# Optimization experiments

Measured on AMD Instinct MI355X. Metric: run time of the kernel, lower is better.

Reference implementation:

```python
import jax, jax.numpy as jnp
import numpy as np

B, C, W, H = 8, 256, 64, 64


def _conv1x1(x, w, b):
    # 1x1 conv == per-pixel channel GEMM. x: [B,C,W,H], w: [O,C], b: [O]
    return jnp.einsum('oc,bchw->bohw', w, x) + b[None, :, None, None]


def setup_inputs() -> dict:
    key = jax.random.key(0)
    ks = jax.random.split(key, 9)
    s = 1.0 / np.sqrt(C)
    return {
        'queries': jax.random.normal(ks[0], (B, C, W, H), dtype=jnp.float32),
        'keys': jax.random.normal(ks[1], (B, C, W, H), dtype=jnp.float32),
        'mask': jax.random.uniform(ks[2], (B, 1, W, H), dtype=jnp.float32),
        'Wq': jax.random.normal(ks[3], (C, C), dtype=jnp.float32) * s,
        'bq': jax.random.normal(ks[4], (C,), dtype=jnp.float32) * 0.01,
        'Wk': jax.random.normal(ks[5], (C, C), dtype=jnp.float32) * s,
        'bk': jax.random.normal(ks[6], (C,), dtype=jnp.float32) * 0.01,
        'Wv': jax.random.normal(ks[7], (C, C), dtype=jnp.float32) * s,
        'bv': jax.random.normal(ks[8], (C,), dtype=jnp.float32) * 0.01,
    }


def reference(queries, keys, mask, Wq, bq, Wk, bk, Wv, bv):
    b, c, w, h = queries.shape
    n = w * h
    q = _conv1x1(queries, Wq, bq).reshape(b, c, n)   # [B,C,N]
    k = _conv1x1(keys, Wk, bk).reshape(b, c, n)      # [B,C,N]
    v = _conv1x1(keys, Wv, bv).reshape(b, c, n)      # [B,C,N]
    # mask spatial size equals feature size -> interpolate(scale_factor=1) is identity
    m = mask.reshape(b, n)                            # [B,N]
    # scores[b,i,j] = <q_i, k_j>; torch's repeated mask multiplies row i by mask[i]
    scores = jnp.einsum('bcq,bck->bqk', q, k) * m[:, :, None]
    attn_w = jax.nn.softmax(scores, axis=-1)          # softmax over key dim
    attn = jnp.einsum('bqk,bck->bcq', attn_w, v).reshape(b, c, w, h)
    return queries * mask + (1.0 - mask) * attn
```

## Files before the change

### kernel.cpp

```cpp
#include <hip/hip_runtime.h>

typedef __attribute__((ext_vector_type(8))) _Float16 half8;
typedef __attribute__((ext_vector_type(4))) _Float16 half4;
typedef __attribute__((ext_vector_type(4))) float f32x4;

#define CDIM 256
#define NDIM 4096
#define MFMAH(a, b, c) __builtin_amdgcn_mfma_f32_16x16x32_f16((a), (b), (c), 0, 0, 0)

__global__ void cast_w_kernel(const float* __restrict__ Wq,
                              const float* __restrict__ Wk,
                              const float* __restrict__ Wv,
                              _Float16* __restrict__ Wc) {
  int t = blockIdx.x * 256 + threadIdx.x;
  int mat = t >> 14;
  int idx = (t & 16383) * 4;
  const float* W = (mat == 0) ? Wq : (mat == 1 ? Wk : Wv);
  float4 w = *(const float4*)(W + idx);
  half4 h = {(_Float16)w.x, (_Float16)w.y, (_Float16)w.z, (_Float16)w.w};
  *(half4*)(Wc + mat * 65536 + idx) = h;
}

__global__ __launch_bounds__(256, 2) void proj_kernel(
    const float* __restrict__ queries, const float* __restrict__ keys,
    const _Float16* __restrict__ Wc,
    const float* __restrict__ bq, const float* __restrict__ bk,
    const float* __restrict__ bv,
    _Float16* __restrict__ Qh, _Float16* __restrict__ Kh,
    _Float16* __restrict__ Vh)
{
  const int z = blockIdx.z, p = z >> 3, b = z & 7;
  const float* __restrict__ X = (p == 0) ? queries : keys;
  const _Float16* __restrict__ W = Wc + p * 65536;
  const float* __restrict__ bias = (p == 0) ? bq : (p == 1 ? bk : bv);
  const int n0 = blockIdx.x * 128;

  __shared__ __align__(16) _Float16 Xs[128][264];

  const int tid = threadIdx.x;
  const int wv = tid >> 6, lane = tid & 63, l16 = lane & 15, quad = lane >> 4;

#pragma unroll
  for (int it = 0; it < 32; ++it) {
    int id = tid + it * 256;
    int c = id >> 5, n4 = id & 31;
    float4 x = *(const float4*)&X[((size_t)(b * CDIM + c)) * NDIM + n0 + n4 * 4];
    Xs[n4 * 4 + 0][c] = (_Float16)x.x;
    Xs[n4 * 4 + 1][c] = (_Float16)x.y;
    Xs[n4 * 4 + 2][c] = (_Float16)x.z;
    Xs[n4 * 4 + 3][c] = (_Float16)x.w;
  }
  __syncthreads();

  f32x4 acc[4][8];
#pragma unroll
  for (int og = 0; og < 4; ++og)
#pragma unroll
    for (int ng = 0; ng < 8; ++ng) acc[og][ng] = (f32x4){0.f, 0.f, 0.f, 0.f};

#pragma unroll
  for (int kc = 0; kc < 8; ++kc) {
    half8 wf[4], xf[8];
#pragma unroll
    for (int og = 0; og < 4; ++og)
      wf[og] = *(const half8*)(W + (wv * 64 + og * 16 + l16) * CDIM + kc * 32 + quad * 8);
#pragma unroll
    for (int ng = 0; ng < 8; ++ng)
      xf[ng] = *(const half8*)&Xs[ng * 16 + l16][kc * 32 + quad * 8];
#pragma unroll
    for (int og = 0; og < 4; ++og)
#pragma unroll
      for (int ng = 0; ng < 8; ++ng)
        acc[og][ng] = MFMAH(wf[og], xf[ng], acc[og][ng]);
  }

#pragma unroll
  for (int og = 0; og < 4; ++og) {
    float4 b4 = *(const float4*)&bias[wv * 64 + og * 16 + quad * 4];
#pragma unroll
    for (int ng = 0; ng < 8; ++ng) {
      const int n = n0 + ng * 16 + l16;
      if (p == 2) {
#pragma unroll
        for (int r = 0; r < 4; ++r) {
          int o = wv * 64 + og * 16 + quad * 4 + r;
          float y = acc[og][ng][r] + ((const float*)&b4)[r];
          Vh[((size_t)(b * CDIM + o)) * NDIM + n] = (_Float16)y;
        }
      } else {
        half4 h4;
#pragma unroll
        for (int r = 0; r < 4; ++r)
          h4[r] = (_Float16)(acc[og][ng][r] + ((const float*)&b4)[r]);
        size_t idx = ((size_t)(b * NDIM + n)) * CDIM + wv * 64 + og * 16 + quad * 4;
        if (p == 0) *(half4*)&Qh[idx] = h4;
        else        *(half4*)&Kh[idx] = h4;
      }
    }
  }
}

__global__ __launch_bounds__(256, 2) void attn_kernel(
    const float* __restrict__ queries, const float* __restrict__ mask,
    const _Float16* __restrict__ Qh, const _Float16* __restrict__ Kh,
    const _Float16* __restrict__ Vh, float* __restrict__ out)
{
  const int blk = blockIdx.x, b = blk & 7, it = blk >> 3;
  const int i0 = it * 64;

  __shared__ __align__(16) _Float16 Ks[64][264];
  __shared__ __align__(16) _Float16 Ps[2][64][72];
  __shared__ __align__(16) float Al[2][64];
  __shared__ __align__(16) float Li[64];

  const int tid = threadIdx.x;
  const int wv = tid >> 6, lane = tid & 63, l16 = lane & 15, quad = lane >> 4;

  half8 qf[8];
  {
    const size_t qrow = ((size_t)(b * NDIM + i0 + wv * 16 + l16)) * CDIM;
#pragma unroll
    for (int kc = 0; kc < 8; ++kc)
      qf[kc] = *(const half8*)(Qh + qrow + kc * 32 + quad * 8);
  }
  const float mval = mask[(size_t)b * NDIM + i0 + wv * 16 + l16];
  float m_run = -1e30f, l_run = 0.f;

  f32x4 O[4][4];
#pragma unroll
  for (int g = 0; g < 4; ++g)
#pragma unroll
    for (int cg = 0; cg < 4; ++cg) O[g][cg] = (f32x4){0.f, 0.f, 0.f, 0.f};

  const _Float16* __restrict__ Kb = Kh + (size_t)b * NDIM * CDIM;
  const _Float16* __restrict__ Vw = Vh + ((size_t)(b * CDIM + wv * 64)) * NDIM;

  for (int jt = 0; jt < 64; ++jt) {
    const int j0 = jt * 64;
    const int pb = jt & 1;
#pragma unroll
    for (int it2 = 0; it2 < 8; ++it2) {
      int id = tid + it2 * 256;
      int j = id >> 5, c8 = id & 31;
      *(uint4*)&Ks[j][c8 * 8] = *(const uint4*)(Kb + (size_t)(j0 + j) * CDIM + c8 * 8);
    }
    half8 vf[2][4];
#pragma unroll
    for (int kk = 0; kk < 2; ++kk)
#pragma unroll
      for (int cg = 0; cg < 4; ++cg)
        vf[kk][cg] = *(const half8*)(Vw + (size_t)(cg * 16 + l16) * NDIM + j0 + kk * 32 + quad * 8);
    __syncthreads();

    f32x4 s[4];
#pragma unroll
    for (int js = 0; js < 4; ++js) s[js] = (f32x4){0.f, 0.f, 0.f, 0.f};
#pragma unroll
    for (int kc = 0; kc < 8; ++kc) {
#pragma unroll
      for (int js = 0; js < 4; ++js) {
        half8 kf = *(const half8*)&Ks[js * 16 + l16][kc * 32 + quad * 8];
        s[js] = MFMAH(kf, qf[kc], s[js]);
      }
    }

    float a[16];
    float mx = -1e30f;
#pragma unroll
    for (int js = 0; js < 4; ++js)
#pragma unroll
      for (int r = 0; r < 4; ++r) {
        float v = s[js][r] * mval;
        a[js * 4 + r] = v;
        mx = fmaxf(mx, v);
      }
    mx = fmaxf(mx, __shfl_xor(mx, 16));
    mx = fmaxf(mx, __shfl_xor(mx, 32));
    const float mnew = fmaxf(m_run, mx);
    const float alpha = __expf(m_run - mnew);
    m_run = mnew;
    float psum = 0.f;
#pragma unroll
    for (int js = 0; js < 4; ++js) {
      float p0 = __expf(a[js * 4 + 0] - mnew);
      float p1 = __expf(a[js * 4 + 1] - mnew);
      float p2 = __expf(a[js * 4 + 2] - mnew);
      float p3 = __expf(a[js * 4 + 3] - mnew);
      psum += (p0 + p1) + (p2 + p3);
      half4 hp = {(_Float16)p0, (_Float16)p1, (_Float16)p2, (_Float16)p3};
      *(half4*)&Ps[pb][wv * 16 + l16][js * 16 + quad * 4] = hp;
    }
    psum += __shfl_xor(psum, 16);
    psum += __shfl_xor(psum, 32);
    l_run = l_run * alpha + psum;
    if (quad == 0) Al[pb][wv * 16 + l16] = alpha;
    __syncthreads();

    f32x4 av[4];
#pragma unroll
    for (int g = 0; g < 4; ++g) av[g] = *(const f32x4*)&Al[pb][g * 16 + quad * 4];
#pragma unroll
    for (int g = 0; g < 4; ++g)
#pragma unroll
      for (int cg = 0; cg < 4; ++cg)
#pragma unroll
        for (int r = 0; r < 4; ++r) O[g][cg][r] *= av[g][r];
#pragma unroll
    for (int kk = 0; kk < 2; ++kk) {
      half8 pa[4];
#pragma unroll
      for (int g = 0; g < 4; ++g)
        pa[g] = *(const half8*)&Ps[pb][g * 16 + l16][kk * 32 + quad * 8];
#pragma unroll
      for (int g = 0; g < 4; ++g)
#pragma unroll
        for (int cg = 0; cg < 4; ++cg)
          O[g][cg] = MFMAH(pa[g], vf[kk][cg], O[g][cg]);
    }
  }

  if (quad == 0) Li[wv * 16 + l16] = 1.0f / l_run;
  __syncthreads();
#pragma unroll
  for (int g = 0; g < 4; ++g) {
    f32x4 li4 = *(const f32x4*)&Li[g * 16 + quad * 4];
    const int i = i0 + g * 16 + quad * 4;
    float4 m4 = *(const float4*)&mask[(size_t)b * NDIM + i];
#pragma unroll
    for (int cg = 0; cg < 4; ++cg) {
      const int c = wv * 64 + cg * 16 + l16;
      const size_t base = ((size_t)(b * CDIM + c)) * NDIM + i;
      float4 q4 = *(const float4*)(queries + base);
      float4 o4;
      o4.x = q4.x * m4.x + (1.f - m4.x) * (O[g][cg][0] * li4[0]);
      o4.y = q4.y * m4.y + (1.f - m4.y) * (O[g][cg][1] * li4[1]);
      o4.z = q4.z * m4.z + (1.f - m4.z) * (O[g][cg][2] * li4[2]);
      o4.w = q4.w * m4.w + (1.f - m4.w) * (O[g][cg][3] * li4[3]);
      *(float4*)(out + base) = o4;
    }
  }
}

extern "C" void kernel_launch(void* const* d_in, const int* in_sizes, int n_in,
                              void* d_out, int out_size, void* d_ws, size_t ws_size,
                              hipStream_t stream) {
  const float* queries = (const float*)d_in[0];
  const float* keys    = (const float*)d_in[1];
  const float* mask    = (const float*)d_in[2];
  const float* Wq = (const float*)d_in[3];
  const float* bq = (const float*)d_in[4];
  const float* Wk = (const float*)d_in[5];
  const float* bk = (const float*)d_in[6];
  const float* Wv = (const float*)d_in[7];
  const float* bv = (const float*)d_in[8];
  float* out = (float*)d_out;

  const size_t elems = (size_t)8 * NDIM * CDIM;
  _Float16* Qh = (_Float16*)d_ws;
  _Float16* Kh = Qh + elems;
  _Float16* Vh = Kh + elems;
  _Float16* Wc = Vh + elems;

  cast_w_kernel<<<dim3(192), 256, 0, stream>>>(Wq, Wk, Wv, Wc);
  proj_kernel<<<dim3(32, 1, 24), 256, 0, stream>>>(
      queries, keys, Wc, bq, bk, bv, Qh, Kh, Vh);
  attn_kernel<<<dim3(512), 256, 0, stream>>>(
      queries, mask, Qh, Kh, Vh, out);
}
```

Before: 331.1 us.

## Switch attention to 32x32x16 MFMA with 2x2 wave split over query and key tiles

Restructures the attention kernel so each wave computes a 32x32 score tile (query half by key half) with 32x32x16 MFMAs. Per-wave row max and sum go through shared memory and are merged across the two key halves, and P is rescaled by each half's factor before the PV MFMA. The softmax uses exp2 with log2e folded into the mask. The intent is fewer MFMA instructions and less redundant K LDS traffic per wave. In exchange it adds extra shared-memory reductions, fp16 rescaling of P, and a scalar, less coalesced output store.

```diff
diff --git a/kernel.cpp b/kernel.cpp
--- a/kernel.cpp
+++ b/kernel.cpp
@@ -3,10 +3,12 @@
 typedef __attribute__((ext_vector_type(8))) _Float16 half8;
 typedef __attribute__((ext_vector_type(4))) _Float16 half4;
 typedef __attribute__((ext_vector_type(4))) float f32x4;
+typedef __attribute__((ext_vector_type(16))) float f32x16;
 
 #define CDIM 256
 #define NDIM 4096
 #define MFMAH(a, b, c) __builtin_amdgcn_mfma_f32_16x16x32_f16((a), (b), (c), 0, 0, 0)
+#define MFMA32(a, b, c) __builtin_amdgcn_mfma_f32_32x32x16_f16((a), (b), (c), 0, 0, 0)
 
 __global__ void cast_w_kernel(const float* __restrict__ Wq,
                               const float* __restrict__ Wk,
@@ -110,27 +112,35 @@
 
   __shared__ __align__(16) _Float16 Ks[64][264];
   __shared__ __align__(16) _Float16 Ps[2][64][72];
-  __shared__ __align__(16) float Al[2][64];
-  __shared__ __align__(16) float Li[64];
+  __shared__ __align__(16) float Mx[2][2][64];
+  __shared__ __align__(16) float Ls[2][2][64];
 
   const int tid = threadIdx.x;
-  const int wv = tid >> 6, lane = tid & 63, l16 = lane & 15, quad = lane >> 4;
-
-  half8 qf[8];
+  const int wv = tid >> 6, lane = tid & 63;
+  const int l32 = lane & 31, hk = lane >> 5;
+  const int wi = wv >> 1, wj = wv & 1;
+
+  const float LOG2E = 1.44269504088896f;
+
+  half8 qf[16];
   {
-    const size_t qrow = ((size_t)(b * NDIM + i0 + wv * 16 + l16)) * CDIM;
-#pragma unroll
-    for (int kc = 0; kc < 8; ++kc)
-      qf[kc] = *(const half8*)(Qh + qrow + kc * 32 + quad * 8);
-  }
-  const float mval = mask[(size_t)b * NDIM + i0 + wv * 16 + l16];
-  float m_run = -1e30f, l_run = 0.f;
-
-  f32x4 O[4][4];
-#pragma unroll
-  for (int g = 0; g < 4; ++g)
-#pragma unroll
-    for (int cg = 0; cg < 4; ++cg) O[g][cg] = (f32x4){0.f, 0.f, 0.f, 0.f};
+    const size_t qrow = ((size_t)(b * NDIM + i0 + wi * 32 + l32)) * CDIM;
+#pragma unroll
+    for (int kc = 0; kc < 16; ++kc)
+      qf[kc] = *(const half8*)(Qh + qrow + kc * 16 + hk * 8);
+  }
+
+  const float mvalL = mask[(size_t)b * NDIM + i0 + wi * 32 + l32] * LOG2E;
+  float m_run[2] = {-1e30f, -1e30f};
+  float l_run[2] = {0.f, 0.f};
+
+  f32x16 O[2][2];
+#pragma unroll
+  for (int t = 0; t < 2; ++t)
+#pragma unroll
+    for (int ct = 0; ct < 2; ++ct)
+#pragma unroll
+      for (int r = 0; r < 16; ++r) O[t][ct][r] = 0.f;
 
   const _Float16* __restrict__ Kb = Kh + (size_t)b * NDIM * CDIM;
   const _Float16* __restrict__ Vw = Vh + ((size_t)(b * CDIM + wv * 64)) * NDIM;
@@ -139,104 +149,98 @@
     const int j0 = jt * 64;
     const int pb = jt & 1;
 #pragma unroll
-    for (int it2 = 0; it2 < 8; ++it2) {
-      int id = tid + it2 * 256;
+    for (int st = 0; st < 8; ++st) {
+      int id = tid + st * 256;
       int j = id >> 5, c8 = id & 31;
       *(uint4*)&Ks[j][c8 * 8] = *(const uint4*)(Kb + (size_t)(j0 + j) * CDIM + c8 * 8);
     }
-    half8 vf[2][4];
-#pragma unroll
-    for (int kk = 0; kk < 2; ++kk)
-#pragma unroll
-      for (int cg = 0; cg < 4; ++cg)
-        vf[kk][cg] = *(const half8*)(Vw + (size_t)(cg * 16 + l16) * NDIM + j0 + kk * 32 + quad * 8);
+    half8 va[2][4];
+#pragma unroll
+    for (int ct = 0; ct < 2; ++ct)
+#pragma unroll
+      for (int js = 0; js < 4; ++js)
+        va[ct][js] = *(const half8*)(Vw + (size_t)(ct * 32 + l32) * NDIM + j0 + js * 16 + hk * 8);
     __syncthreads();
 
-    f32x4 s[4];
-#pragma unroll
-    for (int js = 0; js < 4; ++js) s[js] = (f32x4){0.f, 0.f, 0.f, 0.f};
-#pragma unroll
-    for (int kc = 0; kc < 8; ++kc) {
-#pragma unroll
-      for (int js = 0; js < 4; ++js) {
-        half8 kf = *(const half8*)&Ks[js * 16 + l16][kc * 32 + quad * 8];
-        s[js] = MFMAH(kf, qf[kc], s[js]);
-      }
+    f32x16 s0, s1;
+#pragma unroll
+    for (int r = 0; r < 16; ++r) { s0[r] = 0.f; s1[r] = 0.f; }
+#pragma unroll
+    for (int kc = 0; kc < 16; kc += 2) {
+      half8 kfa = *(const half8*)&Ks[wj * 32 + l32][kc * 16 + hk * 8];
+      half8 kfb = *(const half8*)&Ks[wj * 32 + l32][(kc + 1) * 16 + hk * 8];
+      s0 = MFMA32(kfa, qf[kc], s0);
+      s1 = MFMA32(kfb, qf[kc + 1], s1);
     }
 
     float a[16];
-    float mx = -1e30f;
-#pragma unroll
-    for (int js = 0; js < 4; ++js)
-#pragma unroll
-      for (int r = 0; r < 4; ++r) {
-        float v = s[js][r] * mval;
-        a[js * 4 + r] = v;
-        mx = fmaxf(mx, v);
-      }
-    mx = fmaxf(mx, __shfl_xor(mx, 16));
-    mx = fmaxf(mx, __shfl_xor(mx, 32));
-    const float mnew = fmaxf(m_run, mx);
-    const float alpha = __expf(m_run - mnew);
-    m_run = mnew;
+    float lm = -1e30f;
+#pragma unroll
+    for (int r = 0; r < 16; ++r) {
+      a[r] = (s0[r] + s1[r]) * mvalL;
+      lm = fmaxf(lm, a[r]);
+    }
+    lm = fmaxf(lm, __shfl_xor(lm, 32));
     float psum = 0.f;
 #pragma unroll
-    for (int js = 0; js < 4; ++js) {
-      float p0 = __expf(a[js * 4 + 0] - mnew);
-      float p1 = __expf(a[js * 4 + 1] - mnew);
-      float p2 = __expf(a[js * 4 + 2] - mnew);
-      float p3 = __expf(a[js * 4 + 3] - mnew);
+    for (int rq = 0; rq < 4; ++rq) {
+      float p0 = exp2f(a[rq * 4 + 0] - lm);
+      float p1 = exp2f(a[rq * 4 + 1] - lm);
+      float p2 = exp2f(a[rq * 4 + 2] - lm);
+      float p3 = exp2f(a[rq * 4 + 3] - lm);
       psum += (p0 + p1) + (p2 + p3);
       half4 hp = {(_Float16)p0, (_Float16)p1, (_Float16)p2, (_Float16)p3};
-      *(half4*)&Ps[pb][wv * 16 + l16][js * 16 + quad * 4] = hp;
-    }
-    psum += __shfl_xor(psum, 16);
+      *(half4*)&Ps[pb][wi * 32 + l32][wj * 32 + rq * 8 + hk * 4] = hp;
+    }
     psum += __shfl_xor(psum, 32);
-    l_run = l_run * alpha + psum;
-    if (quad == 0) Al[pb][wv * 16 + l16] = alpha;
+    if (hk == 0) {
+      Mx[pb][wj][wi * 32 + l32] = lm;
+      Ls[pb][wj][wi * 32 + l32] = psum;
+    }
     __syncthreads();
 
-    f32x4 av[4];
-#pragma unroll
-    for (int g = 0; g < 4; ++g) av[g] = *(const f32x4*)&Al[pb][g * 16 + quad * 4];
-#pragma unroll
-    for (int g = 0; g < 4; ++g)
-#pragma unroll
-      for (int cg = 0; cg < 4; ++cg)
-#pragma unroll
-        for (int r = 0; r < 4; ++r) O[g][cg][r] *= av[g][r];
-#pragma unroll
-    for (int kk = 0; kk < 2; ++kk) {
-      half8 pa[4];
-#pragma unroll
-      for (int g = 0; g < 4; ++g)
-        pa[g] = *(const half8*)&Ps[pb][g * 16 + l16][kk * 32 + quad * 8];
-#pragma unroll
-      for (int g = 0; g < 4; ++g)
-#pragma unroll
-        for (int cg = 0; cg < 4; ++cg)
-          O[g][cg] = MFMAH(pa[g], vf[kk][cg], O[g][cg]);
-    }
-  }
-
-  if (quad == 0) Li[wv * 16 + l16] = 1.0f / l_run;
-  __syncthreads();
-#pragma unroll
-  for (int g = 0; g < 4; ++g) {
-    f32x4 li4 = *(const f32x4*)&Li[g * 16 + quad * 4];
-    const int i = i0 + g * 16 + quad * 4;
-    float4 m4 = *(const float4*)&mask[(size_t)b * NDIM + i];
-#pragma unroll
-    for (int cg = 0; cg < 4; ++cg) {
-      const int c = wv * 64 + cg * 16 + l16;
-      const size_t base = ((size_t)(b * CDIM + c)) * NDIM + i;
-      float4 q4 = *(const float4*)(queries + base);
-      float4 o4;
-      o4.x = q4.x * m4.x + (1.f - m4.x) * (O[g][cg][0] * li4[0]);
-      o4.y = q4.y * m4.y + (1.f - m4.y) * (O[g][cg][1] * li4[1]);
-      o4.z = q4.z * m4.z + (1.f - m4.z) * (O[g][cg][2] * li4[2]);
-      o4.w = q4.w * m4.w + (1.f - m4.w) * (O[g][cg][3] * li4[3]);
-      *(float4*)(out + base) = o4;
+#pragma unroll
+    for (int t = 0; t < 2; ++t) {
+      const int irow = t * 32 + l32;
+      const float mx0 = Mx[pb][0][irow];
+      const float mx1 = Mx[pb][1][irow];
+      const float mnew = fmaxf(m_run[t], fmaxf(mx0, mx1));
+      const float alpha = exp2f(m_run[t] - mnew);
+      const float f0 = exp2f(mx0 - mnew);
+      const float f1 = exp2f(mx1 - mnew);
+      l_run[t] = l_run[t] * alpha + Ls[pb][0][irow] * f0 + Ls[pb][1][irow] * f1;
+      m_run[t] = mnew;
+#pragma unroll
+      for (int ct = 0; ct < 2; ++ct)
+#pragma unroll
+        for (int r = 0; r < 16; ++r) O[t][ct][r] *= alpha;
+      const _Float16 hf0 = (_Float16)f0, hf1 = (_Float16)f1;
+#pragma unroll
+      for (int js = 0; js < 4; ++js) {
+        half8 pf = *(const half8*)&Ps[pb][irow][js * 16 + hk * 8];
+        const _Float16 sc = (js < 2) ? hf0 : hf1;
+#pragma unroll
+        for (int e = 0; e < 8; ++e) pf[e] *= sc;
+#pragma unroll
+        for (int ct = 0; ct < 2; ++ct)
+          O[t][ct] = MFMA32(va[ct][js], pf, O[t][ct]);
+      }
+    }
+  }
+
+#pragma unroll
+  for (int t = 0; t < 2; ++t) {
+    const int i = i0 + t * 32 + l32;
+    const float mv = mask[(size_t)b * NDIM + i];
+    const float rl = (1.f - mv) / l_run[t];
+#pragma unroll
+    for (int ct = 0; ct < 2; ++ct) {
+#pragma unroll
+      for (int r = 0; r < 16; ++r) {
+        const int c = wv * 64 + ct * 32 + (r & 3) + 8 * (r >> 2) + 4 * hk;
+        const size_t base = ((size_t)(b * CDIM + c)) * NDIM + i;
+        out[base] = queries[base] * mv + rl * O[t][ct][r];
+      }
     }
   }
 }
```

Result: slower. 348.9 us (+5.4%).

## Prefetch next K tile into registers and swizzle projection LDS staging

Applied to the files above, without the earlier changes.

In the attention loop, the next 64-row K tile is loaded into registers while the current tile is written to shared memory and consumed, so global-load latency overlaps compute. The last iteration wraps around and prefetches tile 0 redundantly. In the projection kernel, the input is staged with four channels per thread and stored as half4 vectors into an XOR-swizzled LDS layout, replacing scalar transposing stores to cut LDS bank conflicts. The reads use the matching swizzle. The register prefetch adds 32 VGPRs per thread, which may lower occupancy.

```diff
diff --git a/kernel.cpp b/kernel.cpp
--- a/kernel.cpp
+++ b/kernel.cpp
@@ -41,14 +41,24 @@
   const int wv = tid >> 6, lane = tid & 63, l16 = lane & 15, quad = lane >> 4;
 
 #pragma unroll
-  for (int it = 0; it < 32; ++it) {
+  for (int it = 0; it < 8; ++it) {
     int id = tid + it * 256;
-    int c = id >> 5, n4 = id & 31;
-    float4 x = *(const float4*)&X[((size_t)(b * CDIM + c)) * NDIM + n0 + n4 * 4];
-    Xs[n4 * 4 + 0][c] = (_Float16)x.x;
-    Xs[n4 * 4 + 1][c] = (_Float16)x.y;
-    Xs[n4 * 4 + 2][c] = (_Float16)x.z;
-    Xs[n4 * 4 + 3][c] = (_Float16)x.w;
+    int n4 = id & 31, c0 = (id >> 5) * 4;
+    const float* Xp = &X[((size_t)(b * CDIM + c0)) * NDIM + n0 + n4 * 4];
+    float4 x0 = *(const float4*)(Xp);
+    float4 x1 = *(const float4*)(Xp + NDIM);
+    float4 x2 = *(const float4*)(Xp + 2 * NDIM);
+    float4 x3 = *(const float4*)(Xp + 3 * NDIM);
+    const int cs = c0 ^ ((n4 & 7) << 3);
+    half4 h;
+    h = (half4){(_Float16)x0.x, (_Float16)x1.x, (_Float16)x2.x, (_Float16)x3.x};
+    *(half4*)&Xs[n4 * 4 + 0][cs] = h;
+    h = (half4){(_Float16)x0.y, (_Float16)x1.y, (_Float16)x2.y, (_Float16)x3.y};
+    *(half4*)&Xs[n4 * 4 + 1][cs] = h;
+    h = (half4){(_Float16)x0.z, (_Float16)x1.z, (_Float16)x2.z, (_Float16)x3.z};
+    *(half4*)&Xs[n4 * 4 + 2][cs] = h;
+    h = (half4){(_Float16)x0.w, (_Float16)x1.w, (_Float16)x2.w, (_Float16)x3.w};
+    *(half4*)&Xs[n4 * 4 + 3][cs] = h;
   }
   __syncthreads();
 
@@ -65,8 +75,10 @@
     for (int og = 0; og < 4; ++og)
       wf[og] = *(const half8*)(W + (wv * 64 + og * 16 + l16) * CDIM + kc * 32 + quad * 8);
 #pragma unroll
-    for (int ng = 0; ng < 8; ++ng)
-      xf[ng] = *(const half8*)&Xs[ng * 16 + l16][kc * 32 + quad * 8];
+    for (int ng = 0; ng < 8; ++ng) {
+      const int row = ng * 16 + l16;
+      xf[ng] = *(const half8*)&Xs[row][(kc * 32 + quad * 8) ^ (((row >> 2) & 7) << 3)];
+    }
 #pragma unroll
     for (int og = 0; og < 4; ++og)
 #pragma unroll
@@ -135,14 +147,29 @@
   const _Float16* __restrict__ Kb = Kh + (size_t)b * NDIM * CDIM;
   const _Float16* __restrict__ Vw = Vh + ((size_t)(b * CDIM + wv * 64)) * NDIM;
 
+  uint4 kreg[8];
+#pragma unroll
+  for (int st = 0; st < 8; ++st) {
+    int id = tid + st * 256;
+    int j = id >> 5, c8 = id & 31;
+    kreg[st] = *(const uint4*)(Kb + (size_t)j * CDIM + c8 * 8);
+  }
+
   for (int jt = 0; jt < 64; ++jt) {
     const int j0 = jt * 64;
     const int pb = jt & 1;
 #pragma unroll
-    for (int it2 = 0; it2 < 8; ++it2) {
-      int id = tid + it2 * 256;
+    for (int st = 0; st < 8; ++st) {
+      int id = tid + st * 256;
       int j = id >> 5, c8 = id & 31;
-      *(uint4*)&Ks[j][c8 * 8] = *(const uint4*)(Kb + (size_t)(j0 + j) * CDIM + c8 * 8);
+      *(uint4*)&Ks[j][c8 * 8] = kreg[st];
+    }
+    const int jn = ((jt + 1) & 63) * 64;
+#pragma unroll
+    for (int st = 0; st < 8; ++st) {
+      int id = tid + st * 256;
+      int j = id >> 5, c8 = id & 31;
+      kreg[st] = *(const uint4*)(Kb + (size_t)(jn + j) * CDIM + c8 * 8);
     }
     half8 vf[2][4];
 #pragma unroll
```

Measured after the change: 550.6 us. +66.3%, slower.
